# Performance work log

Hardware: AMD Instinct MI355X
Metric: run time of the kernel (lower is better)

## Reference

```python
import jax, jax.numpy as jnp
import numpy as np

ENCODED_DIM = 64
NUM_ENCODED = 512
BETA = 0.25


def setup_inputs() -> dict:
    key = jax.random.key(0)
    k1, k2 = jax.random.split(key)
    inputs = jax.random.normal(k1, (32, 64, 64, ENCODED_DIM), dtype=jnp.float32)
    # tf.random_uniform_initializer default: U[-0.05, 0.05]
    codebook = jax.random.uniform(k2, (ENCODED_DIM, NUM_ENCODED), dtype=jnp.float32,
                                  minval=-0.05, maxval=0.05)
    return {"inputs": inputs, "codebook": codebook}


def reference(inputs, codebook):
    original_shape = inputs.shape
    flat = inputs.reshape(-1, ENCODED_DIM)  # [N, D]
    # Squared Euclidean distances to each codebook column: [N, K]
    norms = (jnp.sum(flat ** 2, axis=1, keepdims=True)
             + jnp.sum(codebook ** 2, axis=0)
             - 2.0 * flat @ codebook)
    idx = jnp.argmin(norms, axis=1)  # [N]
    # one_hot @ codebook.T is exactly a row-gather of codebook.T
    quantized = jnp.take(codebook.T, idx, axis=0).reshape(original_shape)
    quantized_loss = jnp.mean((quantized - jax.lax.stop_gradient(inputs)) ** 2)
    commitment_loss = jnp.mean((jax.lax.stop_gradient(quantized) - inputs) ** 2)
    loss = BETA * commitment_loss + quantized_loss
    out = inputs + jax.lax.stop_gradient(quantized - inputs)
    return out, loss
```

## Files before the change

kernel.cpp:

```cpp
#include <hip/hip_runtime.h>
#include <math.h>

#define D 64
#define K 512
#define ROWS 131072
#define NELEM (ROWS * D)
#define TGAP 64.0f
#define FLAGBIT (1 << 30)

typedef _Float16 half8 __attribute__((ext_vector_type(8)));
typedef float floatx4 __attribute__((ext_vector_type(4)));


__global__ __launch_bounds__(512) void vq_setup(const float* __restrict__ cb,
                                                _Float16* __restrict__ gH,
                                                _Float16* __restrict__ gL,
                                                float* __restrict__ Bn) {
    int idx = blockIdx.x * 512 + threadIdx.x;
    int k = idx >> 9, n = idx & 511;
    float c = cb[idx];
    float t = c * 4096.0f;
    _Float16 ch = (_Float16)t;
    float r = t - (float)ch;
    _Float16 cl = (_Float16)(r * 4096.0f);
    int off = (((n >> 4) * 2 + (k >> 5)) * 64 + ((k >> 3) & 3) * 16 + (n & 15)) * 8 + (k & 7);
    gH[off] = ch;
    gL[off] = cl;
    if (blockIdx.x == 0) {
#pragma clang fp contract(off)
        int j = threadIdx.x;
        float b = 0.f;
        for (int kk = 0; kk < D; ++kk) { float cc = cb[kk * K + j]; b = b + cc * cc; }
        Bn[j] = b * 0x1p20f;
    }
}

__global__ __launch_bounds__(256, 2) void vq_main(const float* __restrict__ x,
                                                  const float* __restrict__ cb,
                                                  const _Float16* __restrict__ gH,
                                                  const _Float16* __restrict__ gL,
                                                  const float* __restrict__ Bn,
                                                  float* __restrict__ out,
                                                  double* __restrict__ loss_acc,
                                                  unsigned int* __restrict__ bitmap) {
    __shared__ float ldsB[K];
    __shared__ int rowinfo[4][64];
    __shared__ unsigned int flagbits[8];
    __shared__ float wavesum[4];

    const int tid = threadIdx.x;
    const int lane = tid & 63;
    const int w = tid >> 6;
    const int quad = lane >> 4;
    const int nn = lane & 15;

    ldsB[tid] = Bn[tid];
    ldsB[tid + 256] = Bn[tid + 256];
    if (tid < 8) flagbits[tid] = 0;

    const int rowBase = blockIdx.x * 256 + w * 64;

    half8 xh[4][2], xl[4][2];
    #pragma unroll
    for (int tt = 0; tt < 4; ++tt) {
        #pragma unroll
        for (int s = 0; s < 2; ++s) {
            const float* xp = x + (size_t)(rowBase + tt * 16 + nn) * D + s * 32 + quad * 8;
            float4 v0 = *(const float4*)xp;
            float4 v1 = *(const float4*)(xp + 4);
            float vv[8] = {v0.x, v0.y, v0.z, v0.w, v1.x, v1.y, v1.z, v1.w};
            #pragma unroll
            for (int j = 0; j < 8; ++j) {
                float t = vv[j] * 256.0f;
                _Float16 h = (_Float16)t;
                float r = t - (float)h;
                xh[tt][s][j] = h;
                xl[tt][s][j] = (_Float16)(r * 4096.0f);
            }
        }
    }
    __syncthreads();

    float m1[4][4], m2[4][4];
    int   i1[4][4];
    #pragma unroll
    for (int tt = 0; tt < 4; ++tt)
        #pragma unroll
        for (int r = 0; r < 4; ++r) { m1[tt][r] = INFINITY; m2[tt][r] = INFINITY; i1[tt][r] = 0; }

    const half8* bHp = (const half8*)gH;
    const half8* bLp = (const half8*)gL;

    #pragma unroll 2
    for (int t = 0; t < 32; ++t) {
        half8 bh0 = bHp[(t * 2 + 0) * 64 + lane];
        half8 bl0 = bLp[(t * 2 + 0) * 64 + lane];
        half8 bh1 = bHp[(t * 2 + 1) * 64 + lane];
        half8 bl1 = bLp[(t * 2 + 1) * 64 + lane];
        int col = t * 16 + nn;
        float Bj = ldsB[col];
        #pragma unroll
        for (int tt = 0; tt < 4; ++tt) {
            floatx4 a1 = {0.f, 0.f, 0.f, 0.f};
            floatx4 a2 = {0.f, 0.f, 0.f, 0.f};
            a2 = __builtin_amdgcn_mfma_f32_16x16x32_f16(xl[tt][0], bh0, a2, 0, 0, 0);
            a2 = __builtin_amdgcn_mfma_f32_16x16x32_f16(xh[tt][0], bl0, a2, 0, 0, 0);
            a1 = __builtin_amdgcn_mfma_f32_16x16x32_f16(xh[tt][0], bh0, a1, 0, 0, 0);
            a2 = __builtin_amdgcn_mfma_f32_16x16x32_f16(xl[tt][1], bh1, a2, 0, 0, 0);
            a2 = __builtin_amdgcn_mfma_f32_16x16x32_f16(xh[tt][1], bl1, a2, 0, 0, 0);
            a1 = __builtin_amdgcn_mfma_f32_16x16x32_f16(xh[tt][1], bh1, a1, 0, 0, 0);
            #pragma unroll
            for (int r = 0; r < 4; ++r) {
                float macc = fmaf(0x1p-12f, a2[r], a1[r]);
                float g = fmaf(-2.0f, macc, Bj);
                float old1 = m1[tt][r];
                bool c1 = g < old1;
                m2[tt][r] = fminf(fmaxf(g, old1), m2[tt][r]);
                m1[tt][r] = c1 ? g : old1;
                i1[tt][r] = c1 ? col : i1[tt][r];
            }
        }
    }

    #pragma unroll
    for (int dlt = 1; dlt < 16; dlt <<= 1) {
        #pragma unroll
        for (int tt = 0; tt < 4; ++tt)
            #pragma unroll
            for (int r = 0; r < 4; ++r) {
                float om1 = __shfl_xor(m1[tt][r], dlt);
                int   oi1 = __shfl_xor(i1[tt][r], dlt);
                float om2 = __shfl_xor(m2[tt][r], dlt);
                bool ofirst = (om1 < m1[tt][r]) || (om1 == m1[tt][r] && oi1 < i1[tt][r]);
                float l1   = ofirst ? m1[tt][r] : om1;
                float cand = ofirst ? om2 : m2[tt][r];
                m1[tt][r] = ofirst ? om1 : m1[tt][r];
                i1[tt][r] = ofirst ? oi1 : i1[tt][r];
                m2[tt][r] = fminf(cand, l1);
            }
    }

    if (nn == 0) {
        #pragma unroll
        for (int tt = 0; tt < 4; ++tt)
            #pragma unroll
            for (int r = 0; r < 4; ++r) {
                int rl = tt * 16 + quad * 4 + r;
                bool flg = (m2[tt][r] - m1[tt][r]) < TGAP;
                rowinfo[w][rl] = i1[tt][r] | (flg ? FLAGBIT : 0);
                if (flg) atomicOr(&flagbits[(w * 64 + rl) >> 5], 1u << ((w * 64 + rl) & 31));
            }
    }
    __syncthreads();
    if (tid < 8) bitmap[blockIdx.x * 8 + tid] = flagbits[tid];

    float lsum = 0.f;
    #pragma unroll
    for (int tt = 0; tt < 4; ++tt) {
        #pragma unroll
        for (int p = 0; p < 4; ++p) {
            int rl = tt * 16 + p * 4 + quad;
            int info = rowinfo[w][rl];
            if (!(info & FLAGBIT)) {
                int j = info & 511;
                int kb = nn * 4;
                float q0 = cb[(kb + 0) * K + j];
                float q1 = cb[(kb + 1) * K + j];
                float q2 = cb[(kb + 2) * K + j];
                float q3 = cb[(kb + 3) * K + j];
                size_t row = (size_t)rowBase + rl;
                float4 xv = *(const float4*)(x + row * D + kb);
                float e0 = q0 - xv.x, e1 = q1 - xv.y, e2 = q2 - xv.z, e3 = q3 - xv.w;
                lsum += e0 * e0 + e1 * e1 + e2 * e2 + e3 * e3;
                *(float4*)(out + row * D + kb) = make_float4(q0, q1, q2, q3);
            }
        }
    }
    #pragma unroll
    for (int off = 32; off > 0; off >>= 1) lsum += __shfl_down(lsum, off);
    if (lane == 0) wavesum[w] = lsum;
    __syncthreads();
    if (tid == 0) {
        double tot = (double)wavesum[0] + (double)wavesum[1]
                   + (double)wavesum[2] + (double)wavesum[3];
        atomicAdd(loss_acc, tot);
    }
}

__global__ __launch_bounds__(256) void vq_rescan(const float* __restrict__ x,
                                                 const float* __restrict__ cb,
                                                 float* __restrict__ out,
                                                 double* __restrict__ loss_acc,
                                                 const unsigned int* __restrict__ bitmap) {
#pragma clang fp contract(off)
    const int lane = threadIdx.x & 63;
    const int gwave = blockIdx.x * 4 + (threadIdx.x >> 6);

    unsigned int w0 = bitmap[gwave * 2 + 0];
    unsigned int w1 = bitmap[gwave * 2 + 1];
    unsigned long long mask = ((unsigned long long)w1 << 32) | w0;
    float wloss = 0.f;
    if (mask) {
        float bn[8];
        #pragma unroll
        for (int m = 0; m < 8; ++m) bn[m] = 0.f;
        for (int k = 0; k < D; ++k) {
            const float* crow = cb + k * K + lane;
            #pragma unroll
            for (int m = 0; m < 8; ++m) {
                float c = crow[m * 64];
                bn[m] = bn[m] + c * c;
            }
        }
        while (mask) {
            int b = __builtin_ctzll(mask);
            mask &= mask - 1;
            int row = gwave * 64 + b;
            const float* xr = x + (size_t)row * D;
            float A0;
            {
                float rr[8];
                #pragma unroll
                for (int l = 0; l < 8; ++l) rr[l] = xr[l] * xr[l];
                #pragma unroll
                for (int m = 1; m < 8; ++m)
                    #pragma unroll
                    for (int l = 0; l < 8; ++l) {
                        float q = xr[8 * m + l] * xr[8 * m + l];
                        rr[l] = rr[l] + q;
                    }
                A0 = ((rr[0] + rr[1]) + (rr[2] + rr[3])) + ((rr[4] + rr[5]) + (rr[6] + rr[7]));
            }
            float a[8];
            #pragma unroll
            for (int m = 0; m < 8; ++m) a[m] = 0.f;
            for (int k = 0; k < D; ++k) {
                float xk = xr[k];
                const float* crow = cb + k * K + lane;
                #pragma unroll
                for (int m = 0; m < 8; ++m)
                    a[m] = fmaf(xk, crow[m * 64], a[m]);
            }
            float db = INFINITY; int jb = 0x7fffffff;
            #pragma unroll
            for (int m = 0; m < 8; ++m) {
                float s = A0 + bn[m];
                float t2 = 2.0f * a[m];
                float d = s - t2;
                int j = lane + (m << 6);
                if (d < db) { db = d; jb = j; }
            }
            for (int s = 1; s < 64; s <<= 1) {
                float od = __shfl_xor(db, s);
                int oj = __shfl_xor(jb, s);
                if ((od < db) || (od == db && oj < jb)) { db = od; jb = oj; }
            }
            float q = cb[lane * K + jb];
            out[(size_t)row * D + lane] = q;
            float e = q - xr[lane];
            wloss += e * e;
        }
    }
    #pragma unroll
    for (int off = 32; off > 0; off >>= 1) wloss += __shfl_down(wloss, off);
    if (lane == 0 && wloss != 0.f) atomicAdd(loss_acc, (double)wloss);
}

__global__ void vq_finalize(const double* __restrict__ acc, float* __restrict__ out) {
    out[NELEM] = (float)(acc[0] * (1.25 / (double)NELEM));
}

extern "C" void kernel_launch(void* const* d_in, const int* in_sizes, int n_in,
                              void* d_out, int out_size, void* d_ws, size_t ws_size,
                              hipStream_t stream) {
    const float* x  = (const float*)d_in[0];
    const float* cb = (const float*)d_in[1];
    float* out = (float*)d_out;
    double* loss_acc = (double*)d_ws;
    float* Bn        = (float*)((char*)d_ws + 4096);
    _Float16* gH     = (_Float16*)((char*)d_ws + 8192);
    _Float16* gL     = (_Float16*)((char*)d_ws + 73728);
    unsigned int* bm = (unsigned int*)((char*)d_ws + 139264);

    hipMemsetAsync(d_ws, 0, 16, stream);
    vq_setup<<<64, 512, 0, stream>>>(cb, gH, gL, Bn);
    vq_main<<<ROWS / 256, 256, 0, stream>>>(x, cb, gH, gL, Bn, out, loss_acc, bm);
    vq_rescan<<<512, 256, 0, stream>>>(x, cb, out, loss_acc, bm);
    vq_finalize<<<1, 1, 0, stream>>>(loss_acc, out);
}
```

Baseline: 179.1 us.

## Fuse rescan and finalize into main kernel, halve rows per block

The exact-fp32 rescan of ambiguous rows now runs inside the main kernel per wave, and a last-block ticket writes the final loss. This drops the rescan and finalize launches, the bitmap round trip and the memset, which now happens in the setup kernel. Rows per block go from 256 to 128 with launch bounds allowing 4 blocks per SM. The Bj and -2 scaling are folded into the MFMA accumulator init and the input scale. The risk is that each wave must recompute the codebook norms whenever it has a flagged row, and divergence in those waves can stall the rest of the block.

```diff
diff --git a/kernel.cpp b/kernel.cpp
--- a/kernel.cpp
+++ b/kernel.cpp
@@ -7,6 +7,8 @@
 #define NELEM (ROWS * D)
 #define TGAP 64.0f
 #define FLAGBIT (1 << 30)
+#define RPB 128
+#define NBLK (ROWS / RPB)
 
 typedef _Float16 half8 __attribute__((ext_vector_type(8)));
 typedef float floatx4 __attribute__((ext_vector_type(4)));
@@ -15,7 +17,8 @@
 __global__ __launch_bounds__(512) void vq_setup(const float* __restrict__ cb,
                                                 _Float16* __restrict__ gH,
                                                 _Float16* __restrict__ gL,
-                                                float* __restrict__ Bn) {
+                                                float* __restrict__ Bn,
+                                                unsigned long long* __restrict__ zws) {
     int idx = blockIdx.x * 512 + threadIdx.x;
     int k = idx >> 9, n = idx & 511;
     float c = cb[idx];
@@ -26,6 +29,7 @@
     int off = (((n >> 4) * 2 + (k >> 5)) * 64 + ((k >> 3) & 3) * 16 + (n & 15)) * 8 + (k & 7);
     gH[off] = ch;
     gL[off] = cl;
+    if (blockIdx.x == 1 && threadIdx.x < 4) zws[threadIdx.x] = 0ull;
     if (blockIdx.x == 0) {
 #pragma clang fp contract(off)
         int j = threadIdx.x;
@@ -35,17 +39,17 @@
     }
 }
 
-__global__ __launch_bounds__(256, 2) void vq_main(const float* __restrict__ x,
+__global__ __launch_bounds__(256, 4) void vq_main(const float* __restrict__ x,
                                                   const float* __restrict__ cb,
                                                   const _Float16* __restrict__ gH,
                                                   const _Float16* __restrict__ gL,
                                                   const float* __restrict__ Bn,
                                                   float* __restrict__ out,
                                                   double* __restrict__ loss_acc,
-                                                  unsigned int* __restrict__ bitmap) {
+                                                  unsigned int* __restrict__ ticket) {
     __shared__ float ldsB[K];
-    __shared__ int rowinfo[4][64];
-    __shared__ unsigned int flagbits[8];
+    __shared__ int rowinfo[4][32];
+    __shared__ unsigned int flagbits[4];
     __shared__ float wavesum[4];
 
     const int tid = threadIdx.x;
@@ -56,13 +60,13 @@
 
     ldsB[tid] = Bn[tid];
     ldsB[tid + 256] = Bn[tid + 256];
-    if (tid < 8) flagbits[tid] = 0;
-
-    const int rowBase = blockIdx.x * 256 + w * 64;
-
-    half8 xh[4][2], xl[4][2];
-    #pragma unroll
-    for (int tt = 0; tt < 4; ++tt) {
+    if (tid < 4) flagbits[tid] = 0;
+
+    const int rowBase = blockIdx.x * RPB + w * 32;
+
+    half8 xh[2][2], xl[2][2];
+    #pragma unroll
+    for (int tt = 0; tt < 2; ++tt) {
         #pragma unroll
         for (int s = 0; s < 2; ++s) {
             const float* xp = x + (size_t)(rowBase + tt * 16 + nn) * D + s * 32 + quad * 8;
@@ -71,7 +75,7 @@
             float vv[8] = {v0.x, v0.y, v0.z, v0.w, v1.x, v1.y, v1.z, v1.w};
             #pragma unroll
             for (int j = 0; j < 8; ++j) {
-                float t = vv[j] * 256.0f;
+                float t = vv[j] * -512.0f;
                 _Float16 h = (_Float16)t;
                 float r = t - (float)h;
                 xh[tt][s][j] = h;
@@ -81,10 +85,10 @@
     }
     __syncthreads();
 
-    float m1[4][4], m2[4][4];
-    int   i1[4][4];
-    #pragma unroll
-    for (int tt = 0; tt < 4; ++tt)
+    float m1[2][4], m2[2][4];
+    int   i1[2][4];
+    #pragma unroll
+    for (int tt = 0; tt < 2; ++tt)
         #pragma unroll
         for (int r = 0; r < 4; ++r) { m1[tt][r] = INFINITY; m2[tt][r] = INFINITY; i1[tt][r] = 0; }
 
@@ -100,8 +104,8 @@
         int col = t * 16 + nn;
         float Bj = ldsB[col];
         #pragma unroll
-        for (int tt = 0; tt < 4; ++tt) {
-            floatx4 a1 = {0.f, 0.f, 0.f, 0.f};
+        for (int tt = 0; tt < 2; ++tt) {
+            floatx4 a1 = {Bj, Bj, Bj, Bj};
             floatx4 a2 = {0.f, 0.f, 0.f, 0.f};
             a2 = __builtin_amdgcn_mfma_f32_16x16x32_f16(xl[tt][0], bh0, a2, 0, 0, 0);
             a2 = __builtin_amdgcn_mfma_f32_16x16x32_f16(xh[tt][0], bl0, a2, 0, 0, 0);
@@ -111,8 +115,7 @@
             a1 = __builtin_amdgcn_mfma_f32_16x16x32_f16(xh[tt][1], bh1, a1, 0, 0, 0);
             #pragma unroll
             for (int r = 0; r < 4; ++r) {
-                float macc = fmaf(0x1p-12f, a2[r], a1[r]);
-                float g = fmaf(-2.0f, macc, Bj);
+                float g = fmaf(0x1p-12f, a2[r], a1[r]);
                 float old1 = m1[tt][r];
                 bool c1 = g < old1;
                 m2[tt][r] = fminf(fmaxf(g, old1), m2[tt][r]);
@@ -125,7 +128,7 @@
     #pragma unroll
     for (int dlt = 1; dlt < 16; dlt <<= 1) {
         #pragma unroll
-        for (int tt = 0; tt < 4; ++tt)
+        for (int tt = 0; tt < 2; ++tt)
             #pragma unroll
             for (int r = 0; r < 4; ++r) {
                 float om1 = __shfl_xor(m1[tt][r], dlt);
@@ -142,21 +145,20 @@
 
     if (nn == 0) {
         #pragma unroll
-        for (int tt = 0; tt < 4; ++tt)
+        for (int tt = 0; tt < 2; ++tt)
             #pragma unroll
             for (int r = 0; r < 4; ++r) {
                 int rl = tt * 16 + quad * 4 + r;
                 bool flg = (m2[tt][r] - m1[tt][r]) < TGAP;
                 rowinfo[w][rl] = i1[tt][r] | (flg ? FLAGBIT : 0);
-                if (flg) atomicOr(&flagbits[(w * 64 + rl) >> 5], 1u << ((w * 64 + rl) & 31));
+                if (flg) atomicOr(&flagbits[w], 1u << rl);
             }
     }
     __syncthreads();
-    if (tid < 8) bitmap[blockIdx.x * 8 + tid] = flagbits[tid];
 
     float lsum = 0.f;
     #pragma unroll
-    for (int tt = 0; tt < 4; ++tt) {
+    for (int tt = 0; tt < 2; ++tt) {
         #pragma unroll
         for (int p = 0; p < 4; ++p) {
             int rl = tt * 16 + p * 4 + quad;
@@ -176,31 +178,10 @@
             }
         }
     }
-    #pragma unroll
-    for (int off = 32; off > 0; off >>= 1) lsum += __shfl_down(lsum, off);
-    if (lane == 0) wavesum[w] = lsum;
-    __syncthreads();
-    if (tid == 0) {
-        double tot = (double)wavesum[0] + (double)wavesum[1]
-                   + (double)wavesum[2] + (double)wavesum[3];
-        atomicAdd(loss_acc, tot);
-    }
-}
-
-__global__ __launch_bounds__(256) void vq_rescan(const float* __restrict__ x,
-                                                 const float* __restrict__ cb,
-                                                 float* __restrict__ out,
-                                                 double* __restrict__ loss_acc,
-                                                 const unsigned int* __restrict__ bitmap) {
+
+    unsigned int fmask = flagbits[w];
+    if (fmask) {
 #pragma clang fp contract(off)
-    const int lane = threadIdx.x & 63;
-    const int gwave = blockIdx.x * 4 + (threadIdx.x >> 6);
-
-    unsigned int w0 = bitmap[gwave * 2 + 0];
-    unsigned int w1 = bitmap[gwave * 2 + 1];
-    unsigned long long mask = ((unsigned long long)w1 << 32) | w0;
-    float wloss = 0.f;
-    if (mask) {
         float bn[8];
         #pragma unroll
         for (int m = 0; m < 8; ++m) bn[m] = 0.f;
@@ -212,10 +193,10 @@
                 bn[m] = bn[m] + c * c;
             }
         }
-        while (mask) {
-            int b = __builtin_ctzll(mask);
-            mask &= mask - 1;
-            int row = gwave * 64 + b;
+        while (fmask) {
+            int b = __builtin_ctz(fmask);
+            fmask &= fmask - 1;
+            int row = rowBase + b;
             const float* xr = x + (size_t)row * D;
             float A0;
             {
@@ -258,16 +239,25 @@
             float q = cb[lane * K + jb];
             out[(size_t)row * D + lane] = q;
             float e = q - xr[lane];
-            wloss += e * e;
-        }
-    }
-    #pragma unroll
-    for (int off = 32; off > 0; off >>= 1) wloss += __shfl_down(wloss, off);
-    if (lane == 0 && wloss != 0.f) atomicAdd(loss_acc, (double)wloss);
-}
-
-__global__ void vq_finalize(const double* __restrict__ acc, float* __restrict__ out) {
-    out[NELEM] = (float)(acc[0] * (1.25 / (double)NELEM));
+            lsum += e * e;
+        }
+    }
+
+    #pragma unroll
+    for (int off = 32; off > 0; off >>= 1) lsum += __shfl_down(lsum, off);
+    if (lane == 0) wavesum[w] = lsum;
+    __syncthreads();
+    if (tid == 0) {
+        double tot = (double)wavesum[0] + (double)wavesum[1]
+                   + (double)wavesum[2] + (double)wavesum[3];
+        atomicAdd(loss_acc, tot);
+        __threadfence();
+        unsigned int my = atomicAdd(ticket, 1u);
+        if (my == (unsigned int)(gridDim.x - 1)) {
+            double total = atomicAdd(loss_acc, 0.0);
+            out[NELEM] = (float)(total * (1.25 / (double)NELEM));
+        }
+    }
 }
 
 extern "C" void kernel_launch(void* const* d_in, const int* in_sizes, int n_in,
@@ -276,15 +266,12 @@
     const float* x  = (const float*)d_in[0];
     const float* cb = (const float*)d_in[1];
     float* out = (float*)d_out;
-    double* loss_acc = (double*)d_ws;
+    double* loss_acc     = (double*)d_ws;
+    unsigned int* ticket = (unsigned int*)((char*)d_ws + 8);
     float* Bn        = (float*)((char*)d_ws + 4096);
     _Float16* gH     = (_Float16*)((char*)d_ws + 8192);
     _Float16* gL     = (_Float16*)((char*)d_ws + 73728);
-    unsigned int* bm = (unsigned int*)((char*)d_ws + 139264);
-
-    hipMemsetAsync(d_ws, 0, 16, stream);
-    vq_setup<<<64, 512, 0, stream>>>(cb, gH, gL, Bn);
-    vq_main<<<ROWS / 256, 256, 0, stream>>>(x, cb, gH, gL, Bn, out, loss_acc, bm);
-    vq_rescan<<<512, 256, 0, stream>>>(x, cb, out, loss_acc, bm);
-    vq_finalize<<<1, 1, 0, stream>>>(loss_acc, out);
+
+    vq_setup<<<64, 512, 0, stream>>>(cb, gH, gL, Bn, (unsigned long long*)d_ws);
+    vq_main<<<NBLK, 256, 0, stream>>>(x, cb, gH, gL, Bn, out, loss_acc, ticket);
 }
```

New measurement: 206.7 us. 15.4% more time.
